# Optimization experiments

Measured on AMD Instinct MI355X. Metric: run time of the kernel, lower is better.

## Reference

```python
import jax, jax.numpy as jnp
import numpy as np
import math

NUM_HEAD = 4
GROUPS = 32
EPS = 1e-5


def setup_inputs() -> dict:
    key = jax.random.key(0)
    k1, k2, k3 = jax.random.split(key, 3)
    B, C, H, W = 2, 256, 64, 64
    x = jax.random.normal(k1, (B, C, H, W), dtype=jnp.float32)
    gn_w = jnp.ones((C,), dtype=jnp.float32)
    gn_b = jnp.zeros((C,), dtype=jnp.float32)
    # scaling_init 'u' with scale=1: bound = sqrt(3*2/(fan_in+fan_out))
    fan = (C + 3 * C) / 2
    bound_qkv = math.sqrt(3.0 / fan)
    qkv_w = jax.random.uniform(k2, (3 * C, C), dtype=jnp.float32, minval=-bound_qkv, maxval=bound_qkv)
    bound_o = math.sqrt(3e-10 / C)
    o_w = jax.random.uniform(k3, (C, C), dtype=jnp.float32, minval=-bound_o, maxval=bound_o)
    o_b = jnp.zeros((C,), dtype=jnp.float32)
    return {"x": x, "gn_w": gn_w, "gn_b": gn_b, "qkv_w": qkv_w, "o_w": o_w, "o_b": o_b}


def _group_norm(x, w, b):
    B, C, H, W = x.shape
    xg = x.reshape(B, GROUPS, C // GROUPS, H, W)
    mean = xg.mean(axis=(2, 3, 4), keepdims=True)
    var = xg.var(axis=(2, 3, 4), keepdims=True)
    xn = ((xg - mean) * jax.lax.rsqrt(var + EPS)).reshape(B, C, H, W)
    return xn * w[None, :, None, None] + b[None, :, None, None]


def reference(x, gn_w, gn_b, qkv_w, o_w, o_b):
    B, C, H, W = x.shape
    hd = C // NUM_HEAD
    S = H * W
    norm = _group_norm(x, gn_w, gn_b)
    # 1x1 conv (no bias) == channel matmul
    qkv = jnp.einsum('oc,bchw->bohw', qkv_w, norm)
    qkv = qkv.reshape(B, NUM_HEAD, 3 * hd, S)
    q, k, v = jnp.split(qkv, 3, axis=2)  # each [B, nh, hd, S]
    scale = 1.0 / math.sqrt(C)  # note: sqrt(C), not sqrt(head_dim), per source
    attn = jnp.einsum('bncs,bnct->bnst', q, k) * scale  # [B, nh, S, S]
    attn = jax.nn.softmax(attn, axis=-1)
    out = jnp.einsum('bnst,bnct->bncs', attn, v).reshape(B, C, H, W)
    out = jnp.einsum('oc,bchw->bohw', o_w, out) + o_b[None, :, None, None]
    return out + x
```

## Files before the change

kernel.cpp:

```cpp
#include <hip/hip_runtime.h>
#include <hip/hip_bf16.h>

typedef __hip_bfloat16 bf16;
typedef short short8 __attribute__((ext_vector_type(8)));
typedef float f32x4 __attribute__((ext_vector_type(4)));

__device__ __forceinline__ float b2f(bf16 v) { return __bfloat162float(v); }

__device__ __forceinline__ unsigned short f2bf(float x) {
  unsigned u = __builtin_bit_cast(unsigned, x);
  unsigned r = u + 0x7fffu + ((u >> 16) & 1u);
  return (unsigned short)(r >> 16);
}
__device__ __forceinline__ unsigned pk2(float a, float b) {
  return (unsigned)f2bf(a) | ((unsigned)f2bf(b) << 16);
}
__device__ __forceinline__ unsigned pk2t(float a, float b) {
  return __builtin_amdgcn_perm(__builtin_bit_cast(unsigned, b),
                               __builtin_bit_cast(unsigned, a), 0x07060302u);
}
__device__ __forceinline__ float rd(const void* p, size_t i, int is32) {
  return is32 ? ((const float*)p)[i] : b2f(((const bf16*)p)[i]);
}
__device__ __forceinline__ float blo(unsigned w) {
  return __builtin_bit_cast(float, w << 16);
}
__device__ __forceinline__ float bhi(unsigned w) {
  return __builtin_bit_cast(float, w & 0xffff0000u);
}
__device__ __forceinline__ float fexp2(float x) {
  return __builtin_amdgcn_exp2f(x);
}

#define CQ 0.09016844005556022f

__global__ void __launch_bounds__(256) detect_kernel(const void* __restrict__ x,
                                                     int* __restrict__ flag) {
  __shared__ int cnt[256];
  const bf16* xb = (const bf16*)x;
  int c = 0;
  for (int i = threadIdx.x; i < 4096; i += 256) {
    float v = fabsf(b2f(xb[2 * i]));
    if (v >= 0.0009765625f && v <= 1024.0f) c++;
  }
  cnt[threadIdx.x] = c;
  __syncthreads();
  for (int off = 128; off > 0; off >>= 1) {
    if (threadIdx.x < off) cnt[threadIdx.x] += cnt[threadIdx.x + off];
    __syncthreads();
  }
  if (threadIdx.x == 0) *flag = (cnt[0] < 2048) ? 1 : 0;
}

__global__ void __launch_bounds__(256) pre1_kernel(
    const void* __restrict__ x, const void* __restrict__ gn_w,
    const void* __restrict__ gn_b, const int* __restrict__ flag,
    float* __restrict__ scale, float* __restrict__ shift,
    short* __restrict__ xT) {
  __shared__ __align__(16) float F[64][72];
  const int t = threadIdx.x;
  const int is32 = *flag;
  if (blockIdx.x < 512) {
    const int bx = blockIdx.x;
    const int b = bx >> 8, rest = bx & 255;
    const int s0 = (rest >> 2) * 64, c0 = (rest & 3) * 64;
    if (is32) {
      const float* xp = (const float*)x;
#pragma unroll
      for (int k = 0; k < 4; k++) {
        int idx = k * 256 + t, cl = idx >> 4, c4 = idx & 15;
        float4 v = *(const float4*)&xp[(size_t)(b * 256 + c0 + cl) * 4096 + s0 +
                                       c4 * 4];
        *(float4*)&F[cl][c4 * 4] = v;
      }
    } else {
      const bf16* xp = (const bf16*)x;
#pragma unroll
      for (int k = 0; k < 2; k++) {
        int idx = k * 256 + t, cl = idx >> 3, c8 = idx & 7;
        uint4 u = *(const uint4*)&xp[(size_t)(b * 256 + c0 + cl) * 4096 + s0 +
                                     c8 * 8];
        float4 f0, f1;
        f0.x = blo(u.x); f0.y = bhi(u.x); f0.z = blo(u.y); f0.w = bhi(u.y);
        f1.x = blo(u.z); f1.y = bhi(u.z); f1.z = blo(u.w); f1.w = bhi(u.w);
        *(float4*)&F[cl][c8 * 8] = f0;
        *(float4*)&F[cl][c8 * 8 + 4] = f1;
      }
    }
    __syncthreads();
#pragma unroll
    for (int k = 0; k < 8; k++) {
      int idx = k * 256 + t;
      int sl = idx >> 5, c2 = (idx & 31) * 2;
      unsigned u = pk2(F[c2][sl], F[c2 + 1][sl]);
      *(unsigned*)&xT[((size_t)b * 4096 + s0 + sl) * 256 + c0 + c2] = u;
    }
  } else {
    const int idx0 = blockIdx.x - 512;
    const int b = idx0 >> 5, g = idx0 & 31;
    const size_t base = (size_t)(b * 256 + g * 8) * 4096;
    float s = 0.f, ss = 0.f;
    if (is32) {
      const float4* p = (const float4*)((const float*)x + base);
      for (int i = t; i < 8192; i += 256) {
        float4 v = p[i];
        s += (v.x + v.y) + (v.z + v.w);
        ss += v.x * v.x + v.y * v.y + v.z * v.z + v.w * v.w;
      }
    } else {
      const uint4* p = (const uint4*)((const bf16*)x + base);
      for (int i = t; i < 4096; i += 256) {
        uint4 u = p[i];
#pragma unroll
        for (int k = 0; k < 4; k++) {
          unsigned w = (&u.x)[k];
          float lo = blo(w), hi = bhi(w);
          s += lo + hi;
          ss += lo * lo + hi * hi;
        }
      }
    }
    float* rs = &F[0][0];
    float* rq = rs + 256;
    rs[t] = s;
    rq[t] = ss;
    __syncthreads();
    for (int off = 128; off > 0; off >>= 1) {
      if (t < off) {
        rs[t] += rs[t + off];
        rq[t] += rq[t + off];
      }
      __syncthreads();
    }
    if (t < 8) {
      const float inv_n = 1.f / 32768.f;
      float mean = rs[0] * inv_n;
      float var = rq[0] * inv_n - mean * mean;
      float rstd = rsqrtf(var + 1e-5f);
      int c = g * 8 + t;
      float sc = rd(gn_w, c, is32) * rstd;
      scale[b * 256 + c] = sc;
      shift[b * 256 + c] = rd(gn_b, c, is32) - mean * sc;
    }
  }
}

__global__ void __launch_bounds__(256) pre2_kernel(
    const void* __restrict__ qkv_w, const void* __restrict__ o_w,
    const void* __restrict__ o_b, const float* __restrict__ scale,
    const float* __restrict__ shift, const int* __restrict__ flag,
    short* __restrict__ W2, float* __restrict__ bias2, short* __restrict__ owb,
    float* __restrict__ obf) {
  const int is32 = *flag;
  if (blockIdx.x < 192) {
    const int b = blockIdx.y;
    const int o = blockIdx.x * 4 + (threadIdx.x >> 6);
    const int lane = threadIdx.x & 63;
    const float f = (o % 192 < 64) ? CQ : 1.0f;
    float w[4], acc = 0.f;
#pragma unroll
    for (int k = 0; k < 4; k++) {
      int c = lane * 4 + k;
      w[k] = rd(qkv_w, (size_t)o * 256 + c, is32);
      acc += w[k] * shift[b * 256 + c];
      w[k] = w[k] * scale[b * 256 + c] * f;
    }
#pragma unroll
    for (int m = 1; m < 64; m <<= 1) acc += __shfl_xor(acc, m);
    if (lane == 0) bias2[b * 768 + o] = acc * f;
    uint2 u;
    u.x = pk2(w[0], w[1]);
    u.y = pk2(w[2], w[3]);
    *(uint2*)&W2[((size_t)b * 768 + o) * 256 + lane * 4] = u;
  } else if (blockIdx.y == 0) {
    int bx = blockIdx.x - 192;
    int i = (bx * 256 + threadIdx.x) * 4;
    uint2 u;
    u.x = pk2(rd(o_w, i, is32), rd(o_w, i + 1, is32));
    u.y = pk2(rd(o_w, i + 2, is32), rd(o_w, i + 3, is32));
    *(uint2*)&owb[i] = u;
    if (bx == 0) obf[threadIdx.x] = rd(o_b, threadIdx.x, is32);
  }
}

__global__ void __launch_bounds__(256) gemm_qkv_kernel(
    const short* __restrict__ xT, const short* __restrict__ W2,
    const float* __restrict__ bias2, short* __restrict__ qT,
    short* __restrict__ kF, short* __restrict__ vF) {
  __shared__ __align__(16) short lds[128 * 72 + 64 * 72];
  short* At = lds;
  short* Bt = lds + 128 * 72;
  const int t = threadIdx.x;
  const int wave = t >> 6, lane = t & 63;
  const int ln = lane & 15, quad = lane >> 4;
  const int s0 = blockIdx.x * 128, by = blockIdx.y, b = blockIdx.z;
  const int o0 = by * 64;
  const short* xg = xT + ((size_t)b * 4096 + s0) * 256;
  const short* wg = W2 + ((size_t)b * 768 + o0) * 256;

  f32x4 acc[2][4];
#pragma unroll
  for (int mt = 0; mt < 2; mt++)
#pragma unroll
    for (int nt = 0; nt < 4; nt++) {
      f32x4 z = {0.f, 0.f, 0.f, 0.f};
      acc[mt][nt] = z;
    }

  for (int kt = 0; kt < 4; kt++) {
    __syncthreads();
    {
      int r = t >> 1, ch = t & 1;
#pragma unroll
      for (int j = 0; j < 4; j++)
        *(uint4*)&At[r * 72 + ch * 32 + j * 8] =
            *(const uint4*)&xg[(size_t)r * 256 + kt * 64 + ch * 32 + j * 8];
    }
    {
      int r = t >> 2, cq = t & 3;
#pragma unroll
      for (int j = 0; j < 2; j++)
        *(uint4*)&Bt[r * 72 + cq * 16 + j * 8] =
            *(const uint4*)&wg[(size_t)r * 256 + kt * 64 + cq * 16 + j * 8];
    }
    __syncthreads();
#pragma unroll
    for (int kd = 0; kd < 2; kd++) {
      short8 a[2], bb[4];
#pragma unroll
      for (int mt = 0; mt < 2; mt++)
        a[mt] = *(const short8*)&At[(wave * 32 + mt * 16 + ln) * 72 + kd * 32 +
                                    quad * 8];
#pragma unroll
      for (int nt = 0; nt < 4; nt++)
        bb[nt] = *(const short8*)&Bt[(nt * 16 + ln) * 72 + kd * 32 + quad * 8];
#pragma unroll
      for (int mt = 0; mt < 2; mt++)
#pragma unroll
        for (int nt = 0; nt < 4; nt++)
          acc[mt][nt] = __builtin_amdgcn_mfma_f32_16x16x32_bf16(
              a[mt], bb[nt], acc[mt][nt], 0, 0, 0);
    }
  }

  const int h = by / 3, seg = by % 3;
  const size_t bh = (size_t)b * 4 + h;
  __syncthreads();
  if (seg != 2) {
    short* T = At;
#pragma unroll
    for (int mt = 0; mt < 2; mt++)
#pragma unroll
      for (int nt = 0; nt < 4; nt++)
#pragma unroll
        for (int r = 0; r < 4; r++)
          T[(wave * 32 + mt * 16 + quad * 4 + r) * 72 + nt * 16 + ln] =
              (short)f2bf(acc[mt][nt][r] + bias2[b * 768 + o0 + nt * 16 + ln]);
    __syncthreads();
    if (seg == 0) {
      short* dst = qT + (bh * 4096 + s0) * 64;
      int r = t >> 1, ch = t & 1;
#pragma unroll
      for (int j = 0; j < 2; j++)
        *(uint4*)&dst[r * 64 + ch * 32 + j * 8] =
            *(const uint4*)&T[r * 72 + ch * 32 + j * 8];
    } else {
      short* dstf = kF + bh * 262144;
#pragma unroll
      for (int c = 0; c < 4; c++) {
        int cid = wave * 4 + c;
        int tile = cid >> 1, kd = cid & 1;
        short8 v =
            *(const short8*)&T[(tile * 16 + ln) * 72 + kd * 32 + quad * 8];
        *(short8*)&dstf[(size_t)((s0 / 16 + tile) * 2 + kd) * 512 + lane * 8] =
            v;
      }
    }
  } else {
    short* T2 = At;
#pragma unroll
    for (int mt = 0; mt < 2; mt++)
#pragma unroll
      for (int nt = 0; nt < 4; nt++) {
        float bv = bias2[b * 768 + o0 + nt * 16 + ln];
        uint2 u;
        u.x = pk2(acc[mt][nt][0] + bv, acc[mt][nt][1] + bv);
        u.y = pk2(acc[mt][nt][2] + bv, acc[mt][nt][3] + bv);
        *(uint2*)&T2[(nt * 16 + ln) * 132 + wave * 32 + mt * 16 + quad * 4] = u;
      }
    __syncthreads();
    short* dstf = vF + bh * 262144;
#pragma unroll
    for (int c = 0; c < 4; c++) {
      int cid = wave * 4 + c;
      int ktl = cid >> 3, rem = cid & 7, dt = rem >> 1, kc = rem & 1;
      short8 v = *(const short8*)&T2[(dt * 16 + ln) * 132 + ktl * 64 + kc * 32 +
                                     quad * 8];
      *(short8*)&dstf[(size_t)(((s0 / 64 + ktl) * 4 + dt) * 2 + kc) * 512 +
                      lane * 8] = v;
    }
  }
}

__global__ void __launch_bounds__(256, 4) flash_kernel(
    const short* __restrict__ qT, const short* __restrict__ kF,
    const short* __restrict__ vF, short* __restrict__ attT) {
  __shared__ float smem[4 * 64 * 20];
  const int t = threadIdx.x;
  const int wave = t >> 6, lane = t & 63;
  const int ln = lane & 15, quad = lane >> 4;
  const int L = blockIdx.x;
  const int bh = L & 7;
  const int b = bh >> 2, h = bh & 3;
  const int q0 = (L >> 3) * 16;

  const short* qg = qT + ((size_t)bh * 4096 + q0) * 64;
  const short* kf = kF + (size_t)bh * 262144 + (size_t)wave * 65536;
  const short* vf = vF + (size_t)bh * 262144 + (size_t)wave * 65536;

  short8 qf[2];
#pragma unroll
  for (int kd = 0; kd < 2; kd++)
    qf[kd] = *(const short8*)&qg[ln * 64 + kd * 32 + quad * 8];

  f32x4 ot[4];
#pragma unroll
  for (int dt = 0; dt < 4; dt++) {
    f32x4 z = {0.f, 0.f, 0.f, 0.f};
    ot[dt] = z;
  }
  float lres = 0.f;

  auto LOADKV = [&](short8(&ka)[2][2], short8(&va)[4], int it) {
    const short* kb = kf + (size_t)(it * 2) * 1024;
#pragma unroll
    for (int ct = 0; ct < 2; ct++)
#pragma unroll
      for (int kd = 0; kd < 2; kd++)
        ka[ct][kd] = *(const short8*)&kb[(ct * 2 + kd) * 512 + lane * 8];
    const short* vb = vf + (size_t)(it >> 1) * 4096;
    const int kc = it & 1;
#pragma unroll
    for (int dt = 0; dt < 4; dt++)
      va[dt] = *(const short8*)&vb[(dt * 2 + kc) * 512 + lane * 8];
  };

  auto STEP = [&](const short8(&ka)[2][2], const short8(&va)[4]) {
    f32x4 st[2];
#pragma unroll
    for (int ct = 0; ct < 2; ct++) {
      f32x4 z = {0.f, 0.f, 0.f, 0.f};
      st[ct] = z;
    }
#pragma unroll
    for (int kd = 0; kd < 2; kd++)
#pragma unroll
      for (int ct = 0; ct < 2; ct++)
        st[ct] = __builtin_amdgcn_mfma_f32_16x16x32_bf16(ka[ct][kd], qf[kd],
                                                         st[ct], 0, 0, 0);
    unsigned pk[2][2];
#pragma unroll
    for (int ct = 0; ct < 2; ct++) {
      float p0 = fexp2(st[ct][0]);
      float p1 = fexp2(st[ct][1]);
      float p2 = fexp2(st[ct][2]);
      float p3 = fexp2(st[ct][3]);
      lres += (p0 + p1) + (p2 + p3);
      pk[ct][0] = pk2t(p0, p1);
      pk[ct][1] = pk2t(p2, p3);
    }
    const int tt = quad >> 1;
    const int qs = (quad & 1) * 2;
    union {
      unsigned u[4];
      short8 s;
    } bu;
    bu.u[0] = (unsigned)__shfl((int)pk[tt][0], qs * 16 + ln);
    bu.u[1] = (unsigned)__shfl((int)pk[tt][1], qs * 16 + ln);
    bu.u[2] = (unsigned)__shfl((int)pk[tt][0], (qs + 1) * 16 + ln);
    bu.u[3] = (unsigned)__shfl((int)pk[tt][1], (qs + 1) * 16 + ln);
#pragma unroll
    for (int dt = 0; dt < 4; dt++)
      ot[dt] = __builtin_amdgcn_mfma_f32_16x16x32_bf16(va[dt], bu.s, ot[dt], 0,
                                                       0, 0);
  };

  short8 kaA[2][2], vaA[4], kaB[2][2], vaB[4];
  LOADKV(kaA, vaA, 0);
#pragma unroll 1
  for (int it = 0; it < 32; it += 2) {
    LOADKV(kaB, vaB, it + 1);
    STEP(kaA, vaA);
    if (it < 30) LOADKV(kaA, vaA, it + 2);
    STEP(kaB, vaB);
  }

  lres += __shfl_xor(lres, 16);
  lres += __shfl_xor(lres, 32);
  float* my = smem + (wave * 64 + lane) * 20;
#pragma unroll
  for (int dt = 0; dt < 4; dt++) *(f32x4*)&my[dt * 4] = ot[dt];
  my[16] = lres;
  __syncthreads();

  {
    float lf = 0.f;
    f32x4 of = {0.f, 0.f, 0.f, 0.f};
#pragma unroll
    for (int w = 0; w < 4; w++) {
      const float* pw = smem + (w * 64 + lane) * 20;
      lf += pw[16];
      f32x4 o = *(const f32x4*)&pw[wave * 4];
#pragma unroll
      for (int r = 0; r < 4; r++) of[r] += o[r];
    }
    float invl = 1.f / lf;
    int s = q0 + ln;
    short* ap =
        attT + ((size_t)b * 4096 + s) * 256 + h * 64 + wave * 16 + quad * 4;
    uint2 u;
    u.x = pk2(of[0] * invl, of[1] * invl);
    u.y = pk2(of[2] * invl, of[3] * invl);
    *(uint2*)ap = u;
  }
}

__global__ void __launch_bounds__(256) gemm_o_kernel(
    const short* __restrict__ owb, const short* __restrict__ attT,
    const float* __restrict__ obf, const void* __restrict__ xres,
    void* __restrict__ out, const int* __restrict__ flag) {
  __shared__ __align__(16) float ldsf[64 * 66];
  short* Bt = (short*)ldsf;
  short* At = Bt + 64 * 72;
  const int t = threadIdx.x;
  const int wave = t >> 6, lane = t & 63;
  const int ln = lane & 15, quad = lane >> 4;
  const int s0 = blockIdx.x * 64, o0 = blockIdx.y * 64, b = blockIdx.z;
  const short* ag = attT + ((size_t)b * 4096 + s0) * 256;

  f32x4 acc[4];
#pragma unroll
  for (int mt = 0; mt < 4; mt++) {
    f32x4 z = {0.f, 0.f, 0.f, 0.f};
    acc[mt] = z;
  }

  for (int kt = 0; kt < 4; kt++) {
    __syncthreads();
    {
      int r = t >> 2, cq = t & 3;
#pragma unroll
      for (int j = 0; j < 2; j++)
        *(uint4*)&Bt[r * 72 + cq * 16 + j * 8] =
            *(const uint4*)&ag[(size_t)r * 256 + kt * 64 + cq * 16 + j * 8];
    }
    {
      int r = t >> 2, cq = t & 3;
#pragma unroll
      for (int j = 0; j < 2; j++)
        *(uint4*)&At[r * 72 + cq * 16 + j * 8] =
            *(const uint4*)&owb[(size_t)(o0 + r) * 256 + kt * 64 + cq * 16 +
                                j * 8];
    }
    __syncthreads();
#pragma unroll
    for (int kd = 0; kd < 2; kd++) {
      short8 a[4];
#pragma unroll
      for (int mt = 0; mt < 4; mt++)
        a[mt] = *(const short8*)&At[(mt * 16 + ln) * 72 + kd * 32 + quad * 8];
      short8 bb =
          *(const short8*)&Bt[(wave * 16 + ln) * 72 + kd * 32 + quad * 8];
#pragma unroll
      for (int mt = 0; mt < 4; mt++)
        acc[mt] = __builtin_amdgcn_mfma_f32_16x16x32_bf16(a[mt], bb, acc[mt],
                                                          0, 0, 0);
    }
  }

  __syncthreads();
#pragma unroll
  for (int mt = 0; mt < 4; mt++)
#pragma unroll
    for (int r = 0; r < 4; r++)
      ldsf[(mt * 16 + quad * 4 + r) * 66 + wave * 16 + ln] = acc[mt][r];
  __syncthreads();

  const int is32 = *flag;
#pragma unroll
  for (int j = 0; j < 4; j++) {
    int ol = j * 16 + (t >> 4);
    int sl = (t & 15) * 4;
    f32x4 v = *(const f32x4*)&ldsf[ol * 66 + sl];
    int o = o0 + ol;
    float bv = obf[o];
    size_t base = ((size_t)b * 256 + o) * 4096 + s0 + sl;
    if (is32) {
      const float4 rr = *(const float4*)&((const float*)xres)[base];
      float4 w;
      w.x = v[0] + bv + rr.x;
      w.y = v[1] + bv + rr.y;
      w.z = v[2] + bv + rr.z;
      w.w = v[3] + bv + rr.w;
      *(float4*)&((float*)out)[base] = w;
    } else {
      const uint2 rr = *(const uint2*)&((const bf16*)xres)[base];
      uint2 w;
      w.x = pk2(v[0] + bv + blo(rr.x), v[1] + bv + bhi(rr.x));
      w.y = pk2(v[2] + bv + blo(rr.y), v[3] + bv + bhi(rr.y));
      *(uint2*)&((bf16*)out)[base] = w;
    }
  }
}

extern "C" void kernel_launch(void* const* d_in, const int* in_sizes, int n_in,
                              void* d_out, int out_size, void* d_ws,
                              size_t ws_size, hipStream_t stream) {
  float* ws = (float*)d_ws;
  int* flag = (int*)ws;
  float* scale = ws + 256;
  float* shift = ws + 768;
  float* bias2 = ws + 1280;
  float* obf = ws + 2816;
  short* owb = (short*)(ws + 3072);
  short* W2 = (short*)(ws + 35840);
  short* xT = (short*)(ws + 232448);
  short* qT = (short*)(ws + 1281024);
  short* kF = (short*)(ws + 2329600);
  short* vF = (short*)(ws + 3378176);
  short* attT = (short*)(ws + 4426752);

  detect_kernel<<<1, 256, 0, stream>>>(d_in[0], flag);
  pre1_kernel<<<576, 256, 0, stream>>>(d_in[0], d_in[1], d_in[2], flag, scale,
                                       shift, xT);
  pre2_kernel<<<dim3(256, 2), 256, 0, stream>>>(d_in[3], d_in[4], d_in[5],
                                                scale, shift, flag, W2, bias2,
                                                owb, obf);
  gemm_qkv_kernel<<<dim3(32, 12, 2), 256, 0, stream>>>(xT, W2, bias2, qT, kF,
                                                       vF);
  flash_kernel<<<2048, 256, 0, stream>>>(qT, kF, vF, attT);
  gemm_o_kernel<<<dim3(64, 4, 2), 256, 0, stream>>>(owb, attT, obf, d_in[0],
                                                    d_out, flag);
}
```

Measured before the change: 175.9 us.

## Split flash kernel work as two query tiles by two KV halves per block

Each flash block now covers 32 query rows instead of 16. Its four waves form a 2x2 grid: two query tiles, each paired with two halves of the key/value sequence, so every wave runs twice as many KV iterations. The cross-wave reduction now combines only two partials per query tile, and the grid is halved. The aim is fewer blocks and less reduction and LDS traffic per query. The cost is that each wave does longer serial work and there are fewer blocks to balance across CUs.

```diff
diff --git a/kernel.cpp b/kernel.cpp
--- a/kernel.cpp
+++ b/kernel.cpp
@@ -312,11 +312,13 @@
   const int L = blockIdx.x;
   const int bh = L & 7;
   const int b = bh >> 2, h = bh & 3;
-  const int q0 = (L >> 3) * 16;
-
-  const short* qg = qT + ((size_t)bh * 4096 + q0) * 64;
-  const short* kf = kF + (size_t)bh * 262144 + (size_t)wave * 65536;
-  const short* vf = vF + (size_t)bh * 262144 + (size_t)wave * 65536;
+  const int q0 = (L >> 3) * 32;
+  const int qt_sel = wave & 1;
+  const int half = wave >> 1;
+
+  const short* qg = qT + ((size_t)bh * 4096 + q0 + qt_sel * 16) * 64;
+  const short* kf = kF + (size_t)bh * 262144 + (size_t)half * 131072;
+  const short* vf = vF + (size_t)bh * 262144 + (size_t)half * 131072;
 
   short8 qf[2];
 #pragma unroll
@@ -388,10 +390,10 @@
   short8 kaA[2][2], vaA[4], kaB[2][2], vaB[4];
   LOADKV(kaA, vaA, 0);
 #pragma unroll 1
-  for (int it = 0; it < 32; it += 2) {
+  for (int it = 0; it < 64; it += 2) {
     LOADKV(kaB, vaB, it + 1);
     STEP(kaA, vaA);
-    if (it < 30) LOADKV(kaA, vaA, it + 2);
+    if (it < 62) LOADKV(kaA, vaA, it + 2);
     STEP(kaB, vaB);
   }
 
@@ -404,24 +406,22 @@
   __syncthreads();
 
   {
-    float lf = 0.f;
-    f32x4 of = {0.f, 0.f, 0.f, 0.f};
-#pragma unroll
-    for (int w = 0; w < 4; w++) {
-      const float* pw = smem + (w * 64 + lane) * 20;
-      lf += pw[16];
-      f32x4 o = *(const f32x4*)&pw[wave * 4];
-#pragma unroll
-      for (int r = 0; r < 4; r++) of[r] += o[r];
-    }
+    const float* pA = smem + ((wave & 1) * 64 + lane) * 20;
+    const float* pB = smem + (((wave & 1) + 2) * 64 + lane) * 20;
+    float lf = pA[16] + pB[16];
     float invl = 1.f / lf;
-    int s = q0 + ln;
-    short* ap =
-        attT + ((size_t)b * 4096 + s) * 256 + h * 64 + wave * 16 + quad * 4;
-    uint2 u;
-    u.x = pk2(of[0] * invl, of[1] * invl);
-    u.y = pk2(of[2] * invl, of[3] * invl);
-    *(uint2*)ap = u;
+    int s = q0 + (wave & 1) * 16 + ln;
+    short* ap = attT + ((size_t)b * 4096 + s) * 256 + h * 64;
+#pragma unroll
+    for (int j = 0; j < 2; j++) {
+      int dt = (wave >> 1) * 2 + j;
+      f32x4 oA = *(const f32x4*)&pA[dt * 4];
+      f32x4 oB = *(const f32x4*)&pB[dt * 4];
+      uint2 u;
+      u.x = pk2((oA[0] + oB[0]) * invl, (oA[1] + oB[1]) * invl);
+      u.y = pk2((oA[2] + oB[2]) * invl, (oA[3] + oB[3]) * invl);
+      *(uint2*)&ap[dt * 16 + quad * 4] = u;
+    }
   }
 }
 
@@ -538,7 +538,7 @@
                                                 owb, obf);
   gemm_qkv_kernel<<<dim3(32, 12, 2), 256, 0, stream>>>(xT, W2, bias2, qT, kF,
                                                        vF);
-  flash_kernel<<<2048, 256, 0, stream>>>(qT, kF, vF, attT);
+  flash_kernel<<<1024, 256, 0, stream>>>(qT, kF, vF, attT);
   gemm_o_kernel<<<dim3(64, 4, 2), 256, 0, stream>>>(owb, attT, obf, d_in[0],
                                                     d_out, flag);
 }
```

New measurement: 174.7 us. No clear change (-0.7%).
